# Kernel optimization log

Hardware: AMD Instinct MI355X
Metric: run time of the kernel (lower is better)

Reference implementation:

```python
import jax, jax.numpy as jnp
import numpy as np

B, S, D, H = 2, 2048, 1024, 16
HD = D // H  # head dim = 64; scale uses sqrt(d_k/num_heads) = sqrt(D/H) since d_k==d_model


def setup_inputs() -> dict:
    key = jax.random.key(0)
    ks = jax.random.split(key, 12)
    s = 1.0 / np.sqrt(D)
    inp = {
        "Q": jax.random.normal(ks[0], (B, S, D), jnp.float32),
        "K": jax.random.normal(ks[1], (B, S, D), jnp.float32),
        "V": jax.random.normal(ks[2], (B, S, D), jnp.float32),
        "mask": jnp.tril(jnp.ones((S, S), jnp.int32))[None, None],  # [1,1,S,S] causal
        "Wq": jax.random.normal(ks[3], (D, D), jnp.float32) * s,
        "bq": jnp.zeros((D,), jnp.float32),
        "Wk": jax.random.normal(ks[4], (D, D), jnp.float32) * s,
        "bk": jnp.zeros((D,), jnp.float32),
        "Wv": jax.random.normal(ks[5], (D, D), jnp.float32) * s,
        "bv": jnp.zeros((D,), jnp.float32),
        "Wo": jax.random.normal(ks[6], (D, D), jnp.float32) * s,
        "bo": jnp.zeros((D,), jnp.float32),
    }
    return inp


def _split_heads(x):
    # [B,S,D] -> [B,H,S,HD]
    b, s, _ = x.shape
    return x.reshape(b, s, H, HD).transpose(0, 2, 1, 3)


def reference(Q, K, V, mask, Wq, bq, Wk, bk, Wv, bv, Wo, bo):
    q = _split_heads(Q @ Wq.T + bq)
    k = _split_heads(K @ Wk.T + bk)
    v = _split_heads(V @ Wv.T + bv)
    scale = 1.0 / jnp.sqrt(jnp.asarray(D / H, q.dtype))  # d_k/num_heads with d_k=d_model
    scores = jnp.einsum('bhqd,bhkd->bhqk', q, k) * scale
    scores = jnp.where(mask == 0, jnp.asarray(-1e9, scores.dtype), scores)
    probs = jax.nn.softmax(scores, axis=-1)
    z = jnp.einsum('bhqk,bhkd->bhqd', probs, v)  # [B,H,S,HD]
    z = z.transpose(0, 2, 1, 3).reshape(Q.shape[0], Q.shape[1], D)
    return z @ Wo.T + bo
```

## Files before the change

kernel.cpp:

```cpp
#include <hip/hip_runtime.h>
#include <hip/hip_bf16.h>

typedef unsigned short u16;
typedef unsigned int u32;
typedef __attribute__((ext_vector_type(2))) unsigned int u32x2;
typedef __attribute__((ext_vector_type(8))) short s16x8;
typedef __attribute__((ext_vector_type(4))) float f32x4;
typedef __attribute__((ext_vector_type(16))) float f32x16;

#define NB 2
#define NH 16
#define NS 2048
#define ND 1024
#define QSCALE 0.1803368801111244f

#define AS1(p) ((const __attribute__((address_space(1))) void*)(p))
#define AS3(p) ((__attribute__((address_space(3))) void*)(p))

__device__ __forceinline__ u16 f2bf(float f) {
  u32 u = __float_as_uint(f);
  u = u + 0x7FFFu + ((u >> 16) & 1u);
  return (u16)(u >> 16);
}

__device__ __forceinline__ float bf2f(u16 h) {
  return __uint_as_float(((u32)h) << 16);
}

__device__ __forceinline__ u32 pkbf(float a, float b) {
  __hip_bfloat162 h = __float22bfloat162_rn(make_float2(a, b));
  union { __hip_bfloat162 h; u32 u; } cv;
  cv.h = h;
  return cv.u;
}

__global__ __launch_bounds__(256) void cvt_kernel(
    const float* __restrict__ q, const float* __restrict__ k,
    const float* __restrict__ v, const float* __restrict__ wq,
    const float* __restrict__ wk, const float* __restrict__ wv,
    const float* __restrict__ wo, u16* __restrict__ Xbf,
    u16* __restrict__ Wbf) {
  const int z = blockIdx.z;
  const float* src;
  u16* dst;
  size_t n;
  const size_t NX = (size_t)4096 * 1024, NW = (size_t)1024 * 1024;
  if (z == 0)      { src = q;  dst = Xbf;          n = NX; }
  else if (z == 1) { src = k;  dst = Xbf + NX;     n = NX; }
  else if (z == 2) { src = v;  dst = Xbf + 2 * NX; n = NX; }
  else if (z == 3) { src = wq; dst = Wbf;          n = NW; }
  else if (z == 4) { src = wk; dst = Wbf + NW;     n = NW; }
  else if (z == 5) { src = wv; dst = Wbf + 2 * NW; n = NW; }
  else             { src = wo; dst = Wbf + 3 * NW; n = NW; }
  const size_t n4 = n >> 2;
  for (size_t i = (size_t)blockIdx.x * 256 + threadIdx.x; i < n4;
       i += (size_t)gridDim.x * 256) {
    float4 a = ((const float4*)src)[i];
    uint2 p;
    p.x = (u32)f2bf(a.x) | ((u32)f2bf(a.y) << 16);
    p.y = (u32)f2bf(a.z) | ((u32)f2bf(a.w) << 16);
    ((uint2*)dst)[i] = p;
  }
}

__global__ __launch_bounds__(256) void gemm_qkv_fast(
    const u16* __restrict__ Xbf, const u16* __restrict__ Wbf,
    const float* __restrict__ bq, const float* __restrict__ bk,
    const float* __restrict__ bv, u16* __restrict__ qh, u16* __restrict__ kh,
    u16* __restrict__ vT) {
  const int which = blockIdx.z;
  const u16* A = Xbf + (size_t)which * 4096 * 1024;
  const u16* B = Wbf + (size_t)which * 1024 * 1024;
  const float* bias = (which == 0) ? bq : (which == 1) ? bk : bv;
  const int m0 = blockIdx.y * 128, n0 = blockIdx.x * 128;
  const int tid = threadIdx.x;
  const int w = tid >> 6, l = tid & 63, lr = l & 15, lg = l >> 4;
  const int wr = (w >> 1) * 64, wc = (w & 1) * 64;

  __shared__ u16 As[128 * 32];
  __shared__ u16 Bs[128 * 32];

  const f32x4 fzero = {0.f, 0.f, 0.f, 0.f};
  f32x4 acc[4][4];
#pragma unroll
  for (int m = 0; m < 4; ++m)
#pragma unroll
    for (int n = 0; n < 4; ++n) acc[m][n] = fzero;

  for (int k0 = 0; k0 < 1024; k0 += 32) {
#pragma unroll
    for (int i = 0; i < 2; ++i) {
      int c = i * 256 + tid;
      int row = c >> 2, k4 = (c & 3) ^ (row & 3);
      const u16* sa = A + (size_t)(m0 + row) * 1024 + k0 + k4 * 8;
      const u16* sb = B + (size_t)(n0 + row) * 1024 + k0 + k4 * 8;
      u16* da = As + (i * 256 + w * 64) * 8;
      u16* db = Bs + (i * 256 + w * 64) * 8;
      __builtin_amdgcn_global_load_lds(AS1(sa), AS3(da), 16, 0, 0);
      __builtin_amdgcn_global_load_lds(AS1(sb), AS3(db), 16, 0, 0);
    }
    __syncthreads();
    s16x8 af[4], bf[4];
#pragma unroll
    for (int m = 0; m < 4; ++m) {
      int row = wr + m * 16 + lr;
      af[m] = *(const s16x8*)(As + row * 32 + ((lg ^ (row & 3)) * 8));
    }
#pragma unroll
    for (int n = 0; n < 4; ++n) {
      int row = wc + n * 16 + lr;
      bf[n] = *(const s16x8*)(Bs + row * 32 + ((lg ^ (row & 3)) * 8));
    }
#pragma unroll
    for (int m = 0; m < 4; ++m)
#pragma unroll
      for (int n = 0; n < 4; ++n)
        acc[m][n] = __builtin_amdgcn_mfma_f32_16x16x32_bf16(af[m], bf[n],
                                                            acc[m][n], 0, 0, 0);
    __syncthreads();
  }

#pragma unroll
  for (int m = 0; m < 4; ++m) {
#pragma unroll
    for (int n = 0; n < 4; ++n) {
#pragma unroll
      for (int i = 0; i < 4; ++i) {
        int row = m0 + wr + m * 16 + 4 * lg + i;
        int col = n0 + wc + n * 16 + lr;
        float val = acc[m][n][i] + bias[col];
        if (which == 0) val *= QSCALE;
        int bbi = row >> 11, ss = row & 2047;
        int hhd = col >> 6, hd = col & 63;
        if (which == 0) {
          qh[(((size_t)bbi * NH + hhd) * NS + ss) * 64 + hd] = f2bf(val);
        } else if (which == 1) {
          kh[(((size_t)bbi * NH + hhd) * NS + ss) * 64 + hd] = f2bf(val);
        } else {
          vT[(((size_t)bbi * NH + hhd) * 64 + hd) * NS + ss] = f2bf(val);
        }
      }
    }
  }
}

__global__ __launch_bounds__(256) void gemm_out_fast(
    const u16* __restrict__ zin, const u16* __restrict__ Wbf,
    const float* __restrict__ bo, float* __restrict__ out) {
  const u16* B = Wbf + (size_t)3 * 1024 * 1024;
  const int m0 = blockIdx.y * 128, n0 = blockIdx.x * 128;
  const int tid = threadIdx.x;
  const int w = tid >> 6, l = tid & 63, lr = l & 15, lg = l >> 4;
  const int wr = (w >> 1) * 64, wc = (w & 1) * 64;

  __shared__ u16 As[128 * 32];
  __shared__ u16 Bs[128 * 32];

  const f32x4 fzero = {0.f, 0.f, 0.f, 0.f};
  f32x4 acc[4][4];
#pragma unroll
  for (int m = 0; m < 4; ++m)
#pragma unroll
    for (int n = 0; n < 4; ++n) acc[m][n] = fzero;

  for (int k0 = 0; k0 < 1024; k0 += 32) {
#pragma unroll
    for (int i = 0; i < 2; ++i) {
      int c = i * 256 + tid;
      int row = c >> 2, k4 = (c & 3) ^ (row & 3);
      const u16* sa = zin + (size_t)(m0 + row) * 1024 + k0 + k4 * 8;
      const u16* sb = B + (size_t)(n0 + row) * 1024 + k0 + k4 * 8;
      u16* da = As + (i * 256 + w * 64) * 8;
      u16* db = Bs + (i * 256 + w * 64) * 8;
      __builtin_amdgcn_global_load_lds(AS1(sa), AS3(da), 16, 0, 0);
      __builtin_amdgcn_global_load_lds(AS1(sb), AS3(db), 16, 0, 0);
    }
    __syncthreads();
    s16x8 af[4], bf[4];
#pragma unroll
    for (int m = 0; m < 4; ++m) {
      int row = wr + m * 16 + lr;
      af[m] = *(const s16x8*)(As + row * 32 + ((lg ^ (row & 3)) * 8));
    }
#pragma unroll
    for (int n = 0; n < 4; ++n) {
      int row = wc + n * 16 + lr;
      bf[n] = *(const s16x8*)(Bs + row * 32 + ((lg ^ (row & 3)) * 8));
    }
#pragma unroll
    for (int m = 0; m < 4; ++m)
#pragma unroll
      for (int n = 0; n < 4; ++n)
        acc[m][n] = __builtin_amdgcn_mfma_f32_16x16x32_bf16(af[m], bf[n],
                                                            acc[m][n], 0, 0, 0);
    __syncthreads();
  }

#pragma unroll
  for (int m = 0; m < 4; ++m)
#pragma unroll
    for (int n = 0; n < 4; ++n)
#pragma unroll
      for (int i = 0; i < 4; ++i) {
        int row = m0 + wr + m * 16 + 4 * lg + i;
        int col = n0 + wc + n * 16 + lr;
        out[(size_t)row * 1024 + col] = acc[m][n][i] + bo[col];
      }
}

__device__ __forceinline__ void stage64(const u16* __restrict__ kh,
                                        const u16* __restrict__ vT, int bh,
                                        int t, int tid, int w, u16* kbase,
                                        u16* vbase) {
#pragma unroll
  for (int i = 0; i < 2; ++i) {
    int c = i * 256 + tid;
    int row = c >> 3, k8 = (c & 7) ^ (row & 7);
    const u16* sk = kh + ((size_t)bh * NS + t * 64 + row) * 64 + k8 * 8;
    const u16* sv = vT + ((size_t)bh * 64 + row) * NS + t * 64 + k8 * 8;
    u16* dk = kbase + (i * 256 + w * 64) * 8;
    u16* dv = vbase + (i * 256 + w * 64) * 8;
    __builtin_amdgcn_global_load_lds(AS1(sk), AS3(dk), 16, 0, 0);
    __builtin_amdgcn_global_load_lds(AS1(sv), AS3(dv), 16, 0, 0);
  }
}

__global__ __launch_bounds__(256) void attn_split_kernel(
    const u16* __restrict__ qh, const u16* __restrict__ kh,
    const u16* __restrict__ vT, u16* __restrict__ Opart,
    float* __restrict__ Mpart, float* __restrict__ Lpart) {
  const int f = blockIdx.x;
  const int bh = f & 31;
  const int pp = f >> 5;
  const int bb = bh >> 4;
  (void)bb;
  const int tid = threadIdx.x;
  const int w = tid >> 6, l = tid & 63;
  const int ql = l & 31, hi = l >> 5, hi8 = hi * 8;

  __shared__ u16 smem[2][2][64][64];

#pragma unroll 1
  for (int c = 0; c < 2; ++c) {
    const int band = c ? (15 - pp) : pp;
    const int t0 = c ? (16 - pp) : 0;
    const int t1 = c ? (32 - 2 * pp) : (pp + 1);
    const int q0w = band * 128 + w * 32;

    s16x8 qf[4];
    {
      const u16* qp = qh + ((size_t)bh * NS + q0w + ql) * 64 + hi8;
#pragma unroll
      for (int st = 0; st < 4; ++st) qf[st] = *(const s16x8*)(qp + st * 16);
    }

    f32x16 o0 = {0, 0, 0, 0, 0, 0, 0, 0, 0, 0, 0, 0, 0, 0, 0, 0};
    f32x16 o1 = {0, 0, 0, 0, 0, 0, 0, 0, 0, 0, 0, 0, 0, 0, 0, 0};
    float m_run = -1e30f, l_run = 0.f;

    __syncthreads();
    stage64(kh, vT, bh, t0, tid, w, &smem[t0 & 1][0][0][0],
            &smem[t0 & 1][1][0][0]);
    __syncthreads();

    for (int t = t0; t < t1; ++t) {
      if (t + 1 < t1)
        stage64(kh, vT, bh, t + 1, tid, w, &smem[(t + 1) & 1][0][0][0],
                &smem[(t + 1) & 1][1][0][0]);
      const u16* kp = &smem[t & 1][0][0][0];
      const u16* vp = &smem[t & 1][1][0][0];

#pragma unroll
      for (int sub = 0; sub < 2; ++sub) {
        const int kvg = t * 64 + sub * 32;
        if (kvg > q0w) continue;
        const bool masked = (kvg == q0w);

        const int kr = sub * 32 + ql;
        f32x16 s = {0, 0, 0, 0, 0, 0, 0, 0, 0, 0, 0, 0, 0, 0, 0, 0};
        __builtin_amdgcn_s_setprio(1);
#pragma unroll
        for (int st = 0; st < 4; ++st) {
          s16x8 ak = *(const s16x8*)(kp + kr * 64 +
                                     (((st * 2 + hi) ^ (kr & 7)) * 8));
          s = __builtin_amdgcn_mfma_f32_32x32x16_bf16(ak, qf[st], s, 0, 0, 0);
        }
        __builtin_amdgcn_s_setprio(0);

        float sv_[16];
#pragma unroll
        for (int r = 0; r < 16; ++r) {
          float x = s[r];
          if (masked) {
            int kvloc = (r & 3) + 8 * (r >> 2) + 4 * hi;
            if (kvloc > ql) x = -1e30f;
          }
          sv_[r] = x;
        }

        float m01 = fmaxf(sv_[0], sv_[1]), m23 = fmaxf(sv_[2], sv_[3]);
        float m45 = fmaxf(sv_[4], sv_[5]), m67 = fmaxf(sv_[6], sv_[7]);
        float m89 = fmaxf(sv_[8], sv_[9]), mab = fmaxf(sv_[10], sv_[11]);
        float mcd = fmaxf(sv_[12], sv_[13]), mef = fmaxf(sv_[14], sv_[15]);
        float mx = fmaxf(fmaxf(fmaxf(m01, m23), fmaxf(m45, m67)),
                         fmaxf(fmaxf(m89, mab), fmaxf(mcd, mef)));
        {
          u32x2 rm = __builtin_amdgcn_permlane32_swap(
              __float_as_uint(mx), __float_as_uint(mx), 0, 0);
          mx = fmaxf(__uint_as_float(rm.x), __uint_as_float(rm.y));
        }

        if (__any(mx > m_run)) {
          float mnew = fmaxf(m_run, mx);
          float fs = __builtin_amdgcn_exp2f(m_run - mnew);
#pragma unroll
          for (int r = 0; r < 16; ++r) {
            o0[r] *= fs;
            o1[r] *= fs;
          }
          l_run *= fs;
          m_run = mnew;
        }

        float ps = 0.f;
        u32 pk[8];
#pragma unroll
        for (int tt = 0; tt < 8; ++tt) {
          float a = __builtin_amdgcn_exp2f(sv_[2 * tt] - m_run);
          float b = __builtin_amdgcn_exp2f(sv_[2 * tt + 1] - m_run);
          ps += a + b;
          pk[tt] = pkbf(a, b);
        }
        {
          u32x2 rp = __builtin_amdgcn_permlane32_swap(
              __float_as_uint(ps), __float_as_uint(ps), 0, 0);
          ps = __uint_as_float(rp.x) + __uint_as_float(rp.y);
        }
        l_run += ps;

        u32x2 e0 = __builtin_amdgcn_permlane32_swap(pk[0], pk[2], 0, 0);
        u32x2 e1 = __builtin_amdgcn_permlane32_swap(pk[1], pk[3], 0, 0);
        u32x2 e2 = __builtin_amdgcn_permlane32_swap(pk[4], pk[6], 0, 0);
        u32x2 e3 = __builtin_amdgcn_permlane32_swap(pk[5], pk[7], 0, 0);
        union { u32 u[4]; s16x8 h; } pf0, pf1;
        pf0.u[0] = e0.x; pf0.u[1] = e1.x; pf0.u[2] = e0.y; pf0.u[3] = e1.y;
        pf1.u[0] = e2.x; pf1.u[1] = e3.x; pf1.u[2] = e2.y; pf1.u[3] = e3.y;

        __builtin_amdgcn_s_setprio(1);
#pragma unroll
        for (int k2 = 0; k2 < 2; ++k2) {
          s16x8 pa = (k2 == 0) ? pf0.h : pf1.h;
          int ch = sub * 4 + k2 * 2 + hi;
          s16x8 av0 = *(const s16x8*)(vp + ql * 64 + ((ch ^ (ql & 7)) * 8));
          s16x8 av1 =
              *(const s16x8*)(vp + (32 + ql) * 64 + ((ch ^ (ql & 7)) * 8));
          o0 = __builtin_amdgcn_mfma_f32_32x32x16_bf16(av0, pa, o0, 0, 0, 0);
          o1 = __builtin_amdgcn_mfma_f32_32x32x16_bf16(av1, pa, o1, 0, 0, 0);
        }
        __builtin_amdgcn_s_setprio(0);
      }
      __syncthreads();
    }

    u16* Zw = &smem[0][0][0][0] + w * (32 * 72);
#pragma unroll
    for (int r = 0; r < 16; r += 2) {
      int d0 = (r & 3) + 8 * (r >> 2) + 4 * hi;
      *(u32*)&Zw[ql * 72 + d0]      = pkbf(o0[r], o0[r + 1]);
      *(u32*)&Zw[ql * 72 + 32 + d0] = pkbf(o1[r], o1[r + 1]);
    }
    if (hi == 0) {
      size_t mix = ((size_t)c * 32 + bh) * NS + q0w + ql;
      Mpart[mix] = m_run;
      Lpart[mix] = l_run;
    }
#pragma unroll
    for (int i = 0; i < 4; ++i) {
      int cid = i * 64 + l;
      int row = cid >> 3, c8 = (cid & 7) * 8;
      s16x8 vv = *(const s16x8*)&Zw[row * 72 + c8];
      *(s16x8*)(Opart + (((size_t)c * 32 + bh) * NS + q0w + row) * 64 + c8) =
          vv;
    }
  }
}

__global__ __launch_bounds__(256) void attn_combine_kernel(
    const u16* __restrict__ Opart, const float* __restrict__ Mpart,
    const float* __restrict__ Lpart, u16* __restrict__ z) {
  const int tok = blockIdx.x;
  const int bb = tok >> 11, ss = tok & 2047;
  const int t = threadIdx.x;
  const int d4 = t * 4;
  const int hh = d4 >> 6;
  const size_t qix = ((size_t)bb * NH + hh) * NS + ss;
  const size_t stride = (size_t)32 * NS;

  float m0 = Mpart[qix], l0 = Lpart[qix];
  float m1 = Mpart[qix + stride], l1 = Lpart[qix + stride];
  float mm = fmaxf(m0, m1);
  float w0 = __builtin_amdgcn_exp2f(m0 - mm);
  float w1 = __builtin_amdgcn_exp2f(m1 - mm);
  float inv = 1.f / (w0 * l0 + w1 * l1);
  w0 *= inv;
  w1 *= inv;

  size_t ob = qix * 64 + (d4 & 63);
  uint2 a = *(const uint2*)(Opart + ob);
  uint2 b = *(const uint2*)(Opart + ob + stride * 64);

  float z0 = bf2f((u16)(a.x & 0xffff)) * w0 + bf2f((u16)(b.x & 0xffff)) * w1;
  float z1 = bf2f((u16)(a.x >> 16)) * w0 + bf2f((u16)(b.x >> 16)) * w1;
  float z2 = bf2f((u16)(a.y & 0xffff)) * w0 + bf2f((u16)(b.y & 0xffff)) * w1;
  float z3 = bf2f((u16)(a.y >> 16)) * w0 + bf2f((u16)(b.y >> 16)) * w1;

  uint2 p;
  p.x = pkbf(z0, z1);
  p.y = pkbf(z2, z3);
  *(uint2*)(z + ((size_t)bb * NS + ss) * ND + d4) = p;
}

__global__ __launch_bounds__(128) void attn_kernel(
    const u16* __restrict__ qh, const u16* __restrict__ kh,
    const u16* __restrict__ vT, u16* __restrict__ z) {
  const int f = blockIdx.x;
  const int bh = f & 31;
  const int j0 = (f >> 5) & 7;
  const int g = f >> 8;
  const int mb = 2 * j0;
  const int m =
      (g == 0) ? mb : (g == 1) ? mb + 1 : (g == 2) ? 30 - mb : 31 - mb;
  const int bb = bh >> 4, hh = bh & 15;
  const int tid = threadIdx.x;
  const int w = tid >> 6, l = tid & 63;
  const int ql = l & 31, hi = l >> 5, hi8 = hi * 8;
  const int q0w = m * 64 + w * 32;

  __shared__ u16 smem[2][2][64][64];

  s16x8 qf[4];
  {
    const u16* qp = qh + ((size_t)bh * NS + q0w + ql) * 64 + hi8;
#pragma unroll
    for (int st = 0; st < 4; ++st) qf[st] = *(const s16x8*)(qp + st * 16);
  }

  f32x16 o0 = {0, 0, 0, 0, 0, 0, 0, 0, 0, 0, 0, 0, 0, 0, 0, 0};
  f32x16 o1 = {0, 0, 0, 0, 0, 0, 0, 0, 0, 0, 0, 0, 0, 0, 0, 0};
  float m_run = -1e30f, l_run = 0.f;

  const int ntiles = m + 1;

#pragma unroll
  for (int i = 0; i < 4; ++i) {
    int c = i * 128 + tid;
    int row = c >> 3, k8 = (c & 7) ^ (row & 7);
    const u16* sk = kh + ((size_t)bh * NS + row) * 64 + k8 * 8;
    const u16* sv = vT + ((size_t)bh * 64 + row) * NS + k8 * 8;
    u16* dk = &smem[0][0][0][0] + (i * 128 + w * 64) * 8;
    u16* dv = &smem[0][1][0][0] + (i * 128 + w * 64) * 8;
    __builtin_amdgcn_global_load_lds(AS1(sk), AS3(dk), 16, 0, 0);
    __builtin_amdgcn_global_load_lds(AS1(sv), AS3(dv), 16, 0, 0);
  }
  __syncthreads();

  for (int t = 0; t < ntiles; ++t) {
    if (t + 1 < ntiles) {
      int b1 = (t + 1) & 1;
#pragma unroll
      for (int i = 0; i < 4; ++i) {
        int c = i * 128 + tid;
        int row = c >> 3, k8 = (c & 7) ^ (row & 7);
        const u16* sk =
            kh + ((size_t)bh * NS + (t + 1) * 64 + row) * 64 + k8 * 8;
        const u16* sv =
            vT + ((size_t)bh * 64 + row) * NS + (t + 1) * 64 + k8 * 8;
        u16* dk = &smem[b1][0][0][0] + (i * 128 + w * 64) * 8;
        u16* dv = &smem[b1][1][0][0] + (i * 128 + w * 64) * 8;
        __builtin_amdgcn_global_load_lds(AS1(sk), AS3(dk), 16, 0, 0);
        __builtin_amdgcn_global_load_lds(AS1(sv), AS3(dv), 16, 0, 0);
      }
    }
    const u16* kp = &smem[t & 1][0][0][0];
    const u16* vp = &smem[t & 1][1][0][0];

#pragma unroll
    for (int sub = 0; sub < 2; ++sub) {
      const int kvg = t * 64 + sub * 32;
      if (kvg > q0w) continue;
      const bool masked = (kvg == q0w);

      const int kr = sub * 32 + ql;
      f32x16 s = {0, 0, 0, 0, 0, 0, 0, 0, 0, 0, 0, 0, 0, 0, 0, 0};
#pragma unroll
      for (int st = 0; st < 4; ++st) {
        s16x8 ak = *(const s16x8*)(kp + kr * 64 +
                                   (((st * 2 + hi) ^ (kr & 7)) * 8));
        s = __builtin_amdgcn_mfma_f32_32x32x16_bf16(ak, qf[st], s, 0, 0, 0);
      }

      float sv_[16];
#pragma unroll
      for (int r = 0; r < 16; ++r) {
        float x = s[r];
        if (masked) {
          int kvloc = (r & 3) + 8 * (r >> 2) + 4 * hi;
          if (kvloc > ql) x = -1e30f;
        }
        sv_[r] = x;
      }

      float mx = sv_[0];
#pragma unroll
      for (int r = 1; r < 16; ++r) mx = fmaxf(mx, sv_[r]);
      {
        u32x2 rm = __builtin_amdgcn_permlane32_swap(__float_as_uint(mx),
                                                    __float_as_uint(mx), 0, 0);
        mx = fmaxf(__uint_as_float(rm.x), __uint_as_float(rm.y));
      }

      if (__any(mx > m_run)) {
        float mnew = fmaxf(m_run, mx);
        float fs = __builtin_amdgcn_exp2f(m_run - mnew);
#pragma unroll
        for (int r = 0; r < 16; ++r) {
          o0[r] *= fs;
          o1[r] *= fs;
        }
        l_run *= fs;
        m_run = mnew;
      }

      float ps = 0.f;
      u32 pk[8];
#pragma unroll
      for (int tt = 0; tt < 8; ++tt) {
        float a = __builtin_amdgcn_exp2f(sv_[2 * tt] - m_run);
        float b = __builtin_amdgcn_exp2f(sv_[2 * tt + 1] - m_run);
        ps += a + b;
        pk[tt] = pkbf(a, b);
      }
      {
        u32x2 rp = __builtin_amdgcn_permlane32_swap(__float_as_uint(ps),
                                                    __float_as_uint(ps), 0, 0);
        ps = __uint_as_float(rp.x) + __uint_as_float(rp.y);
      }
      l_run += ps;

      u32x2 e0 = __builtin_amdgcn_permlane32_swap(pk[0], pk[2], 0, 0);
      u32x2 e1 = __builtin_amdgcn_permlane32_swap(pk[1], pk[3], 0, 0);
      u32x2 e2 = __builtin_amdgcn_permlane32_swap(pk[4], pk[6], 0, 0);
      u32x2 e3 = __builtin_amdgcn_permlane32_swap(pk[5], pk[7], 0, 0);
      union { u32 u[4]; s16x8 h; } pf0, pf1;
      pf0.u[0] = e0.x; pf0.u[1] = e1.x; pf0.u[2] = e0.y; pf0.u[3] = e1.y;
      pf1.u[0] = e2.x; pf1.u[1] = e3.x; pf1.u[2] = e2.y; pf1.u[3] = e3.y;

#pragma unroll
      for (int k2 = 0; k2 < 2; ++k2) {
        s16x8 pa = (k2 == 0) ? pf0.h : pf1.h;
        int ch = sub * 4 + k2 * 2 + hi;
        s16x8 av0 = *(const s16x8*)(vp + ql * 64 + ((ch ^ (ql & 7)) * 8));
        s16x8 av1 =
            *(const s16x8*)(vp + (32 + ql) * 64 + ((ch ^ (ql & 7)) * 8));
        o0 = __builtin_amdgcn_mfma_f32_32x32x16_bf16(av0, pa, o0, 0, 0, 0);
        o1 = __builtin_amdgcn_mfma_f32_32x32x16_bf16(av1, pa, o1, 0, 0, 0);
      }
    }
    __syncthreads();
  }

  float inv = 1.f / l_run;
  u16* Zw = &smem[0][0][0][0] + w * (32 * 72);
#pragma unroll
  for (int r = 0; r < 16; r += 2) {
    int d0 = (r & 3) + 8 * (r >> 2) + 4 * hi;
    *(u32*)&Zw[ql * 72 + d0]      = pkbf(o0[r] * inv, o0[r + 1] * inv);
    *(u32*)&Zw[ql * 72 + 32 + d0] = pkbf(o1[r] * inv, o1[r + 1] * inv);
  }
#pragma unroll
  for (int i = 0; i < 4; ++i) {
    int cid = i * 64 + l;
    int row = cid >> 3, c8 = (cid & 7) * 8;
    s16x8 vv = *(const s16x8*)&Zw[row * 72 + c8];
    *(s16x8*)(z + ((size_t)bb * NS + q0w + row) * ND + hh * 64 + c8) = vv;
  }
}

__global__ __launch_bounds__(256) void proj_qkv_kernel(
    const float* __restrict__ Qin, const float* __restrict__ Kin,
    const float* __restrict__ Vin,
    const float* __restrict__ Wq, const float* __restrict__ bq,
    const float* __restrict__ Wk, const float* __restrict__ bk,
    const float* __restrict__ Wv, const float* __restrict__ bv,
    u16* __restrict__ qh, u16* __restrict__ kh, u16* __restrict__ vT) {
  const int which = blockIdx.z;
  const float* X = (which == 0) ? Qin : (which == 1) ? Kin : Vin;
  const float* W = (which == 0) ? Wq : (which == 1) ? Wk : Wv;
  const float* bias = (which == 0) ? bq : (which == 1) ? bk : bv;

  const int m0 = blockIdx.y * 128, n0 = blockIdx.x * 128;
  const int tid = threadIdx.x;
  const int w = tid >> 6, l = tid & 63, lr = l & 15, lg = l >> 4;
  const int wr = (w >> 1) * 64, wc = (w & 1) * 64;

  __shared__ u16 As[128][40];
  __shared__ u16 Bs[128][40];

  const f32x4 fzero = {0.f, 0.f, 0.f, 0.f};
  f32x4 acc[4][4];
#pragma unroll
  for (int m = 0; m < 4; ++m)
#pragma unroll
    for (int n = 0; n < 4; ++n) acc[m][n] = fzero;

  for (int k0 = 0; k0 < 1024; k0 += 32) {
#pragma unroll
    for (int i = 0; i < 4; ++i) {
      int idx = tid + i * 256;
      int row = idx >> 3, c4 = (idx & 7) * 4;
      float4 a = *(const float4*)(X + (size_t)(m0 + row) * 1024 + k0 + c4);
      *(u32*)&As[row][c4]     = (u32)f2bf(a.x) | ((u32)f2bf(a.y) << 16);
      *(u32*)&As[row][c4 + 2] = (u32)f2bf(a.z) | ((u32)f2bf(a.w) << 16);
      float4 b = *(const float4*)(W + (size_t)(n0 + row) * 1024 + k0 + c4);
      *(u32*)&Bs[row][c4]     = (u32)f2bf(b.x) | ((u32)f2bf(b.y) << 16);
      *(u32*)&Bs[row][c4 + 2] = (u32)f2bf(b.z) | ((u32)f2bf(b.w) << 16);
    }
    __syncthreads();
    s16x8 af[4], bf[4];
#pragma unroll
    for (int m = 0; m < 4; ++m)
      af[m] = *(const s16x8*)&As[wr + m * 16 + lr][lg * 8];
#pragma unroll
    for (int n = 0; n < 4; ++n)
      bf[n] = *(const s16x8*)&Bs[wc + n * 16 + lr][lg * 8];
#pragma unroll
    for (int m = 0; m < 4; ++m)
#pragma unroll
      for (int n = 0; n < 4; ++n)
        acc[m][n] = __builtin_amdgcn_mfma_f32_16x16x32_bf16(af[m], bf[n],
                                                            acc[m][n], 0, 0, 0);
    __syncthreads();
  }

  u16* dst01 = (which == 0) ? qh : kh;
#pragma unroll
  for (int m = 0; m < 4; ++m) {
#pragma unroll
    for (int n = 0; n < 4; ++n) {
#pragma unroll
      for (int i = 0; i < 4; ++i) {
        int row = m0 + wr + m * 16 + 4 * lg + i;
        int col = n0 + wc + n * 16 + lr;
        float val = acc[m][n][i] + bias[col];
        if (which == 0) val *= QSCALE;
        int bbi = row >> 11, ss = row & 2047;
        int hhd = col >> 6, hd = col & 63;
        if (which < 2) {
          dst01[(((size_t)bbi * NH + hhd) * NS + ss) * 64 + hd] = f2bf(val);
        } else {
          vT[(((size_t)bbi * NH + hhd) * 64 + hd) * NS + ss] = f2bf(val);
        }
      }
    }
  }
}

__global__ __launch_bounds__(256) void proj_out_kernel(
    const u16* __restrict__ zin, const float* __restrict__ Wo,
    const float* __restrict__ bo, float* __restrict__ out) {
  const int m0 = blockIdx.y * 128, n0 = blockIdx.x * 128;
  const int tid = threadIdx.x;
  const int w = tid >> 6, l = tid & 63, lr = l & 15, lg = l >> 4;
  const int wr = (w >> 1) * 64, wc = (w & 1) * 64;

  __shared__ u16 As[128][40];
  __shared__ u16 Bs[128][40];

  const f32x4 fzero = {0.f, 0.f, 0.f, 0.f};
  f32x4 acc[4][4];
#pragma unroll
  for (int m = 0; m < 4; ++m)
#pragma unroll
    for (int n = 0; n < 4; ++n) acc[m][n] = fzero;

  for (int k0 = 0; k0 < 1024; k0 += 32) {
#pragma unroll
    for (int i = 0; i < 2; ++i) {
      int idx = tid + i * 256;
      int row = idx >> 2, c8 = (idx & 3) * 8;
      *(s16x8*)&As[row][c8] =
          *(const s16x8*)(zin + (size_t)(m0 + row) * 1024 + k0 + c8);
    }
#pragma unroll
    for (int i = 0; i < 4; ++i) {
      int idx = tid + i * 256;
      int row = idx >> 3, c4 = (idx & 7) * 4;
      float4 b = *(const float4*)(Wo + (size_t)(n0 + row) * 1024 + k0 + c4);
      *(u32*)&Bs[row][c4]     = (u32)f2bf(b.x) | ((u32)f2bf(b.y) << 16);
      *(u32*)&Bs[row][c4 + 2] = (u32)f2bf(b.z) | ((u32)f2bf(b.w) << 16);
    }
    __syncthreads();
    s16x8 af[4], bf[4];
#pragma unroll
    for (int m = 0; m < 4; ++m)
      af[m] = *(const s16x8*)&As[wr + m * 16 + lr][lg * 8];
#pragma unroll
    for (int n = 0; n < 4; ++n)
      bf[n] = *(const s16x8*)&Bs[wc + n * 16 + lr][lg * 8];
#pragma unroll
    for (int m = 0; m < 4; ++m)
#pragma unroll
      for (int n = 0; n < 4; ++n)
        acc[m][n] = __builtin_amdgcn_mfma_f32_16x16x32_bf16(af[m], bf[n],
                                                            acc[m][n], 0, 0, 0);
    __syncthreads();
  }

#pragma unroll
  for (int m = 0; m < 4; ++m)
#pragma unroll
    for (int n = 0; n < 4; ++n)
#pragma unroll
      for (int i = 0; i < 4; ++i) {
        int row = m0 + wr + m * 16 + 4 * lg + i;
        int col = n0 + wc + n * 16 + lr;
        out[(size_t)row * 1024 + col] = acc[m][n][i] + bo[col];
      }
}

extern "C" void kernel_launch(void* const* d_in, const int* in_sizes, int n_in,
                              void* d_out, int out_size, void* d_ws,
                              size_t ws_size, hipStream_t stream) {
  const float* Q = (const float*)d_in[0];
  const float* K = (const float*)d_in[1];
  const float* V = (const float*)d_in[2];
  const float* Wq = (const float*)d_in[4];
  const float* bq = (const float*)d_in[5];
  const float* Wk = (const float*)d_in[6];
  const float* bk = (const float*)d_in[7];
  const float* Wv = (const float*)d_in[8];
  const float* bv = (const float*)d_in[9];
  const float* Wo = (const float*)d_in[10];
  const float* bo = (const float*)d_in[11];
  float* out = (float*)d_out;

  const size_t M1 = (size_t)1024 * 1024;
  u16* base = (u16*)d_ws;

  if (ws_size >= (size_t)58720256) {
    u16* Wbf = base;
    u16* qh = base + 4 * M1;
    u16* zz = qh;
    u16* kh = base + 8 * M1;
    u16* vT = base + 12 * M1;
    u16* Xbf = base + 16 * M1;
    u16* Opart = base + 16 * M1;
    float* Mpart = (float*)(base + 24 * M1);
    float* Lpart = (float*)(base + 24 * M1 + 256 * 1024);

    cvt_kernel<<<dim3(512, 1, 7), 256, 0, stream>>>(Q, K, V, Wq, Wk, Wv, Wo,
                                                    Xbf, Wbf);
    gemm_qkv_fast<<<dim3(8, 32, 3), 256, 0, stream>>>(Xbf, Wbf, bq, bk, bv, qh,
                                                      kh, vT);
    attn_split_kernel<<<dim3(512), 256, 0, stream>>>(qh, kh, vT, Opart, Mpart,
                                                     Lpart);
    attn_combine_kernel<<<dim3(4096), 256, 0, stream>>>(Opart, Mpart, Lpart,
                                                        zz);
    gemm_out_fast<<<dim3(8, 32), 256, 0, stream>>>(zz, Wbf, bo, out);
  } else {
    u16* qh = base;
    u16* kh = base + 4 * M1;
    u16* vT = base + 8 * M1;
    u16* zz = base + 12 * M1;
    proj_qkv_kernel<<<dim3(8, 32, 3), 256, 0, stream>>>(Q, K, V, Wq, bq, Wk,
                                                        bk, Wv, bv, qh, kh, vT);
    attn_kernel<<<dim3(1024), 128, 0, stream>>>(qh, kh, vT, zz);
    proj_out_kernel<<<dim3(8, 32), 256, 0, stream>>>(zz, Wo, bo, out);
  }
}
```

Measured before the change: 140.8 us.

## Process 64-wide KV tiles per softmax step, lazy rescale, rebalance convert grid

The attention inner loop now computes both 32-column score blocks of each 64-key tile before a single max, rescale and exp pass. This halves the per-step reductions and permlane swaps and lets four PV MFMAs issue back to back. The online softmax rescale now fires only when the running max grows by more than 8 (log2 units), which skips many rescales but lets unnormalised values grow up to 2^8. The convert kernel is split into 16 equal 1M-element slices with int indexing so blocks get balanced work. In exchange, the diagonal tile does wasted MFMAs on masked halves and register pressure rises.

```diff
diff --git a/kernel.cpp b/kernel.cpp
--- a/kernel.cpp
+++ b/kernel.cpp
@@ -40,21 +40,19 @@
     const float* __restrict__ wk, const float* __restrict__ wv,
     const float* __restrict__ wo, u16* __restrict__ Xbf,
     u16* __restrict__ Wbf) {
-  const int z = blockIdx.z;
+  const int s = blockIdx.z;
+  const size_t M1 = (size_t)1024 * 1024;
   const float* src;
   u16* dst;
-  size_t n;
-  const size_t NX = (size_t)4096 * 1024, NW = (size_t)1024 * 1024;
-  if (z == 0)      { src = q;  dst = Xbf;          n = NX; }
-  else if (z == 1) { src = k;  dst = Xbf + NX;     n = NX; }
-  else if (z == 2) { src = v;  dst = Xbf + 2 * NX; n = NX; }
-  else if (z == 3) { src = wq; dst = Wbf;          n = NW; }
-  else if (z == 4) { src = wk; dst = Wbf + NW;     n = NW; }
-  else if (z == 5) { src = wv; dst = Wbf + 2 * NW; n = NW; }
-  else             { src = wo; dst = Wbf + 3 * NW; n = NW; }
-  const size_t n4 = n >> 2;
-  for (size_t i = (size_t)blockIdx.x * 256 + threadIdx.x; i < n4;
-       i += (size_t)gridDim.x * 256) {
+  if (s < 4)       { src = q + (size_t)s * M1;        dst = Xbf + (size_t)s * M1; }
+  else if (s < 8)  { src = k + (size_t)(s - 4) * M1;  dst = Xbf + (size_t)s * M1; }
+  else if (s < 12) { src = v + (size_t)(s - 8) * M1;  dst = Xbf + (size_t)s * M1; }
+  else if (s == 12){ src = wq; dst = Wbf; }
+  else if (s == 13){ src = wk; dst = Wbf + M1; }
+  else if (s == 14){ src = wv; dst = Wbf + 2 * M1; }
+  else             { src = wo; dst = Wbf + 3 * M1; }
+  const int n4 = 1024 * 1024 / 4;
+  for (int i = blockIdx.x * 256 + threadIdx.x; i < n4; i += gridDim.x * 256) {
     float4 a = ((const float4*)src)[i];
     uint2 p;
     p.x = (u32)f2bf(a.x) | ((u32)f2bf(a.y) << 16);
@@ -232,8 +230,6 @@
   const int f = blockIdx.x;
   const int bh = f & 31;
   const int pp = f >> 5;
-  const int bb = bh >> 4;
-  (void)bb;
   const int tid = threadIdx.x;
   const int w = tid >> 6, l = tid & 63;
   const int ql = l & 31, hi = l >> 5, hi8 = hi * 8;
@@ -270,47 +266,63 @@
       const u16* kp = &smem[t & 1][0][0][0];
       const u16* vp = &smem[t & 1][1][0][0];
 
-#pragma unroll
-      for (int sub = 0; sub < 2; ++sub) {
-        const int kvg = t * 64 + sub * 32;
-        if (kvg > q0w) continue;
-        const bool masked = (kvg == q0w);
-
-        const int kr = sub * 32 + ql;
-        f32x16 s = {0, 0, 0, 0, 0, 0, 0, 0, 0, 0, 0, 0, 0, 0, 0, 0};
+      const int kvg0 = t * 64, kvg1 = t * 64 + 32;
+      if (kvg0 <= q0w) {
+        f32x16 s0 = {0, 0, 0, 0, 0, 0, 0, 0, 0, 0, 0, 0, 0, 0, 0, 0};
+        f32x16 s1 = {0, 0, 0, 0, 0, 0, 0, 0, 0, 0, 0, 0, 0, 0, 0, 0};
+        const int kr0 = ql, kr1 = 32 + ql;
         __builtin_amdgcn_s_setprio(1);
 #pragma unroll
         for (int st = 0; st < 4; ++st) {
-          s16x8 ak = *(const s16x8*)(kp + kr * 64 +
-                                     (((st * 2 + hi) ^ (kr & 7)) * 8));
-          s = __builtin_amdgcn_mfma_f32_32x32x16_bf16(ak, qf[st], s, 0, 0, 0);
+          s16x8 ak = *(const s16x8*)(kp + kr0 * 64 +
+                                     (((st * 2 + hi) ^ (kr0 & 7)) * 8));
+          s0 = __builtin_amdgcn_mfma_f32_32x32x16_bf16(ak, qf[st], s0, 0, 0, 0);
+        }
+        if (kvg1 <= q0w) {
+#pragma unroll
+          for (int st = 0; st < 4; ++st) {
+            s16x8 ak = *(const s16x8*)(kp + kr1 * 64 +
+                                       (((st * 2 + hi) ^ (kr1 & 7)) * 8));
+            s1 = __builtin_amdgcn_mfma_f32_32x32x16_bf16(ak, qf[st], s1, 0, 0,
+                                                         0);
+          }
         }
         __builtin_amdgcn_s_setprio(0);
 
-        float sv_[16];
-#pragma unroll
-        for (int r = 0; r < 16; ++r) {
-          float x = s[r];
-          if (masked) {
+        if (kvg0 == q0w) {
+#pragma unroll
+          for (int r = 0; r < 16; ++r) {
             int kvloc = (r & 3) + 8 * (r >> 2) + 4 * hi;
-            if (kvloc > ql) x = -1e30f;
+            if (kvloc > ql) s0[r] = -1e30f;
           }
-          sv_[r] = x;
-        }
-
-        float m01 = fmaxf(sv_[0], sv_[1]), m23 = fmaxf(sv_[2], sv_[3]);
-        float m45 = fmaxf(sv_[4], sv_[5]), m67 = fmaxf(sv_[6], sv_[7]);
-        float m89 = fmaxf(sv_[8], sv_[9]), mab = fmaxf(sv_[10], sv_[11]);
-        float mcd = fmaxf(sv_[12], sv_[13]), mef = fmaxf(sv_[14], sv_[15]);
-        float mx = fmaxf(fmaxf(fmaxf(m01, m23), fmaxf(m45, m67)),
-                         fmaxf(fmaxf(m89, mab), fmaxf(mcd, mef)));
+        }
+        if (kvg1 > q0w) {
+#pragma unroll
+          for (int r = 0; r < 16; ++r) s1[r] = -1e30f;
+        } else if (kvg1 == q0w) {
+#pragma unroll
+          for (int r = 0; r < 16; ++r) {
+            int kvloc = (r & 3) + 8 * (r >> 2) + 4 * hi;
+            if (kvloc > ql) s1[r] = -1e30f;
+          }
+        }
+
+        float mr[16];
+#pragma unroll
+        for (int r = 0; r < 16; ++r) mr[r] = fmaxf(s0[r], s1[r]);
+#pragma unroll
+        for (int off = 8; off; off >>= 1)
+#pragma unroll
+          for (int r = 0; r < 8; ++r)
+            if (r < off) mr[r] = fmaxf(mr[r], mr[r + off]);
+        float mx = mr[0];
         {
           u32x2 rm = __builtin_amdgcn_permlane32_swap(
               __float_as_uint(mx), __float_as_uint(mx), 0, 0);
           mx = fmaxf(__uint_as_float(rm.x), __uint_as_float(rm.y));
         }
 
-        if (__any(mx > m_run)) {
+        if (!__all(mx - m_run <= 8.0f)) {
           float mnew = fmaxf(m_run, mx);
           float fs = __builtin_amdgcn_exp2f(m_run - mnew);
 #pragma unroll
@@ -323,13 +335,20 @@
         }
 
         float ps = 0.f;
-        u32 pk[8];
+        u32 pk0[8], pk1[8];
 #pragma unroll
         for (int tt = 0; tt < 8; ++tt) {
-          float a = __builtin_amdgcn_exp2f(sv_[2 * tt] - m_run);
-          float b = __builtin_amdgcn_exp2f(sv_[2 * tt + 1] - m_run);
+          float a = __builtin_amdgcn_exp2f(s0[2 * tt] - m_run);
+          float b = __builtin_amdgcn_exp2f(s0[2 * tt + 1] - m_run);
           ps += a + b;
-          pk[tt] = pkbf(a, b);
+          pk0[tt] = pkbf(a, b);
+        }
+#pragma unroll
+        for (int tt = 0; tt < 8; ++tt) {
+          float a = __builtin_amdgcn_exp2f(s1[2 * tt] - m_run);
+          float b = __builtin_amdgcn_exp2f(s1[2 * tt + 1] - m_run);
+          ps += a + b;
+          pk1[tt] = pkbf(a, b);
         }
         {
           u32x2 rp = __builtin_amdgcn_permlane32_swap(
@@ -338,24 +357,31 @@
         }
         l_run += ps;
 
-        u32x2 e0 = __builtin_amdgcn_permlane32_swap(pk[0], pk[2], 0, 0);
-        u32x2 e1 = __builtin_amdgcn_permlane32_swap(pk[1], pk[3], 0, 0);
-        u32x2 e2 = __builtin_amdgcn_permlane32_swap(pk[4], pk[6], 0, 0);
-        u32x2 e3 = __builtin_amdgcn_permlane32_swap(pk[5], pk[7], 0, 0);
-        union { u32 u[4]; s16x8 h; } pf0, pf1;
-        pf0.u[0] = e0.x; pf0.u[1] = e1.x; pf0.u[2] = e0.y; pf0.u[3] = e1.y;
-        pf1.u[0] = e2.x; pf1.u[1] = e3.x; pf1.u[2] = e2.y; pf1.u[3] = e3.y;
+        u32x2 e0 = __builtin_amdgcn_permlane32_swap(pk0[0], pk0[2], 0, 0);
+        u32x2 e1 = __builtin_amdgcn_permlane32_swap(pk0[1], pk0[3], 0, 0);
+        u32x2 e2 = __builtin_amdgcn_permlane32_swap(pk0[4], pk0[6], 0, 0);
+        u32x2 e3 = __builtin_amdgcn_permlane32_swap(pk0[5], pk0[7], 0, 0);
+        u32x2 e4 = __builtin_amdgcn_permlane32_swap(pk1[0], pk1[2], 0, 0);
+        u32x2 e5 = __builtin_amdgcn_permlane32_swap(pk1[1], pk1[3], 0, 0);
+        u32x2 e6 = __builtin_amdgcn_permlane32_swap(pk1[4], pk1[6], 0, 0);
+        u32x2 e7 = __builtin_amdgcn_permlane32_swap(pk1[5], pk1[7], 0, 0);
+        union { u32 u[4]; s16x8 h; } pf[4];
+        pf[0].u[0] = e0.x; pf[0].u[1] = e1.x; pf[0].u[2] = e0.y; pf[0].u[3] = e1.y;
+        pf[1].u[0] = e2.x; pf[1].u[1] = e3.x; pf[1].u[2] = e2.y; pf[1].u[3] = e3.y;
+        pf[2].u[0] = e4.x; pf[2].u[1] = e5.x; pf[2].u[2] = e4.y; pf[2].u[3] = e5.y;
+        pf[3].u[0] = e6.x; pf[3].u[1] = e7.x; pf[3].u[2] = e6.y; pf[3].u[3] = e7.y;
 
         __builtin_amdgcn_s_setprio(1);
 #pragma unroll
-        for (int k2 = 0; k2 < 2; ++k2) {
-          s16x8 pa = (k2 == 0) ? pf0.h : pf1.h;
-          int ch = sub * 4 + k2 * 2 + hi;
+        for (int ks = 0; ks < 4; ++ks) {
+          int ch = ks * 2 + hi;
           s16x8 av0 = *(const s16x8*)(vp + ql * 64 + ((ch ^ (ql & 7)) * 8));
           s16x8 av1 =
               *(const s16x8*)(vp + (32 + ql) * 64 + ((ch ^ (ql & 7)) * 8));
-          o0 = __builtin_amdgcn_mfma_f32_32x32x16_bf16(av0, pa, o0, 0, 0, 0);
-          o1 = __builtin_amdgcn_mfma_f32_32x32x16_bf16(av1, pa, o1, 0, 0, 0);
+          o0 = __builtin_amdgcn_mfma_f32_32x32x16_bf16(av0, pf[ks].h, o0, 0, 0,
+                                                       0);
+          o1 = __builtin_amdgcn_mfma_f32_32x32x16_bf16(av1, pf[ks].h, o1, 0, 0,
+                                                       0);
         }
         __builtin_amdgcn_s_setprio(0);
       }
@@ -758,8 +784,8 @@
     float* Mpart = (float*)(base + 24 * M1);
     float* Lpart = (float*)(base + 24 * M1 + 256 * 1024);
 
-    cvt_kernel<<<dim3(512, 1, 7), 256, 0, stream>>>(Q, K, V, Wq, Wk, Wv, Wo,
-                                                    Xbf, Wbf);
+    cvt_kernel<<<dim3(128, 1, 16), 256, 0, stream>>>(Q, K, V, Wq, Wk, Wv, Wo,
+                                                     Xbf, Wbf);
     gemm_qkv_fast<<<dim3(8, 32, 3), 256, 0, stream>>>(Xbf, Wbf, bq, bk, bv, qh,
                                                       kh, vT);
     attn_split_kernel<<<dim3(512), 256, 0, stream>>>(qh, kh, vT, Opart, Mpart,
```

New measurement: 137.1 us. -2.6%, faster.
